# Kernel optimization log

Measured on AMD Instinct MI355X. Metric: run time of the kernel, lower is better.

## Reference

```python
import jax, jax.numpy as jnp
import numpy as np

N_USER = 100000
N_ITEM = 100000
N_EDGE = 1600000
IN_U = 128
IN_I = 128
OUT = 64
NEG_SLOPE = 0.01  # torch F.leaky_relu default


def setup_inputs() -> dict:
    key = jax.random.key(0)
    ks = jax.random.split(key, 12)
    return {
        'feat_user': jax.random.normal(ks[0], (N_USER, IN_U), jnp.float32),
        'feat_item': jax.random.normal(ks[1], (N_ITEM, IN_I), jnp.float32),
        'W_user': jax.random.normal(ks[2], (IN_U, OUT), jnp.float32) * 0.05,
        'b_user': jax.random.normal(ks[3], (OUT,), jnp.float32) * 0.05,
        'W_item': jax.random.normal(ks[4], (IN_I, OUT), jnp.float32) * 0.05,
        'b_item': jax.random.normal(ks[5], (OUT,), jnp.float32) * 0.05,
        'attn_w': jax.random.normal(ks[6], (2 * OUT, 1), jnp.float32) * 0.05,
        'src_u2i': jax.random.randint(ks[7], (N_EDGE,), 0, N_USER),
        'dst_u2i': jax.random.randint(ks[8], (N_EDGE,), 0, N_ITEM),
        'src_i2u': jax.random.randint(ks[9], (N_EDGE,), 0, N_ITEM),
        'dst_i2u': jax.random.randint(ks[10], (N_EDGE,), 0, N_USER),
    }


def _segment_softmax(e, seg, num_segments):
    # e: [E], seg: [E] destination ids -> softmax over edges sharing a dst
    m = jax.ops.segment_max(e, seg, num_segments=num_segments)
    ex = jnp.exp(e - m[seg])
    s = jax.ops.segment_sum(ex, seg, num_segments=num_segments)
    return ex / s[seg]


def _etype_aggregate(Wh_src, Wh_dst, attn_w, src, dst, n_dst):
    # gather per-edge src/dst projected features: [E, OUT]
    zs = Wh_src[src]
    zd = Wh_dst[dst]
    # attn([zs || zd]) == zs @ a_src + zd @ a_dst (split the 2*OUT weight)
    a_src, a_dst = attn_w[:OUT, 0], attn_w[OUT:, 0]
    e = zs @ a_src + zd @ a_dst  # [E]
    e = jnp.where(e > 0, e, NEG_SLOPE * e)  # leaky_relu
    alpha = _segment_softmax(e, dst, n_dst)  # [E]
    # weighted scatter-sum into destination nodes
    return jax.ops.segment_sum(alpha[:, None] * zs, dst, num_segments=n_dst)


def reference(feat_user, feat_item, W_user, b_user, W_item, b_item, attn_w,
              src_u2i, dst_u2i, src_i2u, dst_i2u):
    Wh_user = feat_user @ W_user + b_user  # fc['user'] (etype 'user': user->item)
    Wh_item = feat_item @ W_item + b_item  # fc['item'] (etype 'item': item->user)
    # etype 'user': user -> item; dst attention feature is Wh_item on item nodes
    h_item = _etype_aggregate(Wh_user, Wh_item, attn_w, src_u2i, dst_u2i, N_ITEM)
    # etype 'item': item -> user
    h_user = _etype_aggregate(Wh_item, Wh_user, attn_w, src_i2u, dst_i2u, N_USER)
    # update_nodes sums all 'self_*' per ntype; each ntype has exactly one here
    return jnp.concatenate([h_user, h_item], axis=0)  # [N_USER+N_ITEM, OUT]
```

## Files before the change

kernel.cpp:

```cpp
#include <hip/hip_runtime.h>
#include <hip/hip_bf16.h>

#define NU 100000
#define NI 100000
#define NE 1600000
#define KIN 128
#define KOUT 64

#define NCOPY 8
#define PBK 128
#define NP 782
#define CAP2 384
#define CHUNK 4096
#define SRTSZ (NCOPY * CAP2 + PBK * 7)
#define AGG_THREADS 512
#define NWAVE 8

#define LIN_ROWS 64
#define LIN_GRID 512
#define LIN_ITERS 1563

typedef short bf16x8 __attribute__((ext_vector_type(8)));
typedef float f32x4  __attribute__((ext_vector_type(4)));

__device__ __forceinline__ unsigned short f2bf(float f) {
    unsigned u = __float_as_uint(f);
    unsigned r = (u + 0x7fffu + ((u >> 16) & 1u)) >> 16;
    return (unsigned short)r;
}
__device__ __forceinline__ float bf2f(unsigned short h) {
    return __uint_as_float(((unsigned)h) << 16);
}
__device__ __forceinline__ void split_bf16(float f, unsigned short& h, unsigned short& l) {
    h = f2bf(f);
    float r = f - bf2f(h);
    l = f2bf(r);
}

__global__ __launch_bounds__(256) void linear_attn_kernel(
    const float* __restrict__ A0, const float* __restrict__ W0, const float* __restrict__ bv0,
    const float* __restrict__ A1, const float* __restrict__ W1, const float* __restrict__ bv1,
    const float* __restrict__ attn,
    unsigned short* __restrict__ Wh0, float* __restrict__ su0, float* __restrict__ sd0,
    unsigned short* __restrict__ Wh1, float* __restrict__ su1, float* __restrict__ sd1)
{
    __shared__ float Al[LIN_ROWS * 132];
    __shared__ __align__(16) unsigned short Wph[4 * 4 * 64 * 8];
    __shared__ __align__(16) unsigned short Wpl[4 * 4 * 64 * 8];

    int half = gridDim.x >> 1;
    bool second = blockIdx.x >= (unsigned)half;
    const float* A = second ? A1 : A0;
    const float* W = second ? W1 : W0;
    const float* bvec = second ? bv1 : bv0;
    unsigned short* Wh = second ? Wh1 : Wh0;
    float* s_src = second ? su1 : su0;
    float* s_dst = second ? sd1 : sd0;
    int blk = second ? (blockIdx.x - half) : blockIdx.x;

    int t = threadIdx.x;
    int l   = t & 63;
    int wv  = t >> 6;
    int ln  = l & 15;
    int grp = l >> 4;

    for (int i = 0; i < 4; i++) {
        int s = t + 256 * i;
        int sl = s & 63, nt = (s >> 6) & 3, ks = s >> 8;
        int kb = ks * 32 + (sl >> 4) * 8;
        int nn = nt * 16 + (sl & 15);
        int base = ((ks * 4 + nt) * 64 + sl) * 8;
        #pragma unroll
        for (int j = 0; j < 8; j++) {
            unsigned short h, lo2;
            split_bf16(W[(size_t)(kb + j) * KOUT + nn], h, lo2);
            Wph[base + j] = h; Wpl[base + j] = lo2;
        }
    }

    float asl[4], adl[4], bl4[4];
    #pragma unroll
    for (int nt = 0; nt < 4; nt++) {
        asl[nt] = attn[nt * 16 + ln];
        adl[nt] = attn[64 + nt * 16 + ln];
        bl4[nt] = bvec[nt * 16 + ln];
    }

    int arow = wv * 16 + ln;

    for (int c = blk; c < LIN_ITERS; c += half) {
        int rowbase = c * LIN_ROWS;
        __syncthreads();
        for (int g = t; g < LIN_ROWS * 32; g += 256) {
            int rr = g >> 5;
            int q  = g & 31;
            float4 v = {0.f, 0.f, 0.f, 0.f};
            int grow = rowbase + rr;
            if (grow < NU) v = ((const float4*)(A + (size_t)grow * 128))[q];
            *(float4*)&Al[rr * 132 + q * 4] = v;
        }
        __syncthreads();

        f32x4 acc0 = {bl4[0], bl4[0], bl4[0], bl4[0]};
        f32x4 acc1 = {bl4[1], bl4[1], bl4[1], bl4[1]};
        f32x4 acc2 = {bl4[2], bl4[2], bl4[2], bl4[2]};
        f32x4 acc3 = {bl4[3], bl4[3], bl4[3], bl4[3]};

        #pragma unroll
        for (int ks = 0; ks < 4; ks++) {
            int k0 = ks * 32 + grp * 8;
            const float* ap = &Al[arow * 132 + k0];
            float4 va = *(const float4*)ap;
            float4 vb = *(const float4*)(ap + 4);
            float av[8] = {va.x, va.y, va.z, va.w, vb.x, vb.y, vb.z, vb.w};
            bf16x8 ahi, alo;
            #pragma unroll
            for (int j = 0; j < 8; j++) {
                unsigned short h, lo2;
                split_bf16(av[j], h, lo2);
                ahi[j] = (short)h; alo[j] = (short)lo2;
            }
            #pragma unroll
            for (int nt = 0; nt < 4; nt++) {
                bf16x8 bhi8 = *(const bf16x8*)&Wph[((ks * 4 + nt) * 64 + l) * 8];
                bf16x8 blo8 = *(const bf16x8*)&Wpl[((ks * 4 + nt) * 64 + l) * 8];
                f32x4 a = (nt == 0) ? acc0 : (nt == 1) ? acc1 : (nt == 2) ? acc2 : acc3;
                a = __builtin_amdgcn_mfma_f32_16x16x32_bf16(ahi, bhi8, a, 0, 0, 0);
                a = __builtin_amdgcn_mfma_f32_16x16x32_bf16(ahi, blo8, a, 0, 0, 0);
                a = __builtin_amdgcn_mfma_f32_16x16x32_bf16(alo, bhi8, a, 0, 0, 0);
                if (nt == 0) acc0 = a; else if (nt == 1) acc1 = a; else if (nt == 2) acc2 = a; else acc3 = a;
            }
        }

        int growbase = rowbase + wv * 16;
        f32x4 accs[4] = {acc0, acc1, acc2, acc3};
        #pragma unroll
        for (int nt = 0; nt < 4; nt++) {
            #pragma unroll
            for (int r = 0; r < 4; r++) {
                int row = growbase + grp * 4 + r;
                if (row < NU) Wh[(size_t)row * KOUT + nt * 16 + ln] = f2bf(accs[nt][r]);
            }
        }
        #pragma unroll
        for (int r = 0; r < 4; r++) {
            float p1 = accs[0][r] * asl[0] + accs[1][r] * asl[1] + accs[2][r] * asl[2] + accs[3][r] * asl[3];
            float p2 = accs[0][r] * adl[0] + accs[1][r] * adl[1] + accs[2][r] * adl[2] + accs[3][r] * adl[3];
            #pragma unroll
            for (int off = 1; off < 16; off <<= 1) {
                p1 += __shfl_xor(p1, off);
                p2 += __shfl_xor(p2, off);
            }
            int row = growbase + grp * 4 + r;
            if (ln == 0 && row < NU) { s_src[row] = p1; s_dst[row] = p2; }
        }
    }
}

__global__ __launch_bounds__(256) void scatter_kernel(
    const int* __restrict__ src_u2i, const int* __restrict__ dst_u2i,
    const int* __restrict__ src_i2u, const int* __restrict__ dst_i2u,
    int* __restrict__ cur_item, int* __restrict__ cur_user,
    int* __restrict__ ebuf_item, int* __restrict__ ebuf_user,
    int nE, int nbs)
{
    __shared__ int raw[CHUNK];
    __shared__ unsigned short bkt[CHUNK];
    __shared__ int cnt[NP];
    __shared__ int gb[NP];
    __shared__ int lc[NP];

    bool u2i = blockIdx.x < (unsigned)nbs;
    int blk = u2i ? blockIdx.x : (blockIdx.x - nbs);
    int copy = blockIdx.x & (NCOPY - 1);
    const int* src = u2i ? src_u2i : src_i2u;
    const int* dst = u2i ? dst_u2i : dst_i2u;
    int* cur  = (u2i ? cur_item : cur_user) + copy * NP;
    int* ebuf = (u2i ? ebuf_item : ebuf_user) + (size_t)copy * NP * CAP2;

    int t = threadIdx.x;
    for (int i = t; i < NP; i += 256) { cnt[i] = 0; lc[i] = 0; }
    __syncthreads();

    int e0 = blk * CHUNK;
    int n = nE - e0; if (n > CHUNK) n = CHUNK;

    for (int j = t; j < n; j += 256) {
        int s = src[e0 + j], d = dst[e0 + j];
        int b = d >> 7;
        raw[j] = s | ((d & 127) << 17);
        bkt[j] = (unsigned short)b;
        atomicAdd(&cnt[b], 1);
    }
    __syncthreads();

    for (int b = t; b < NP; b += 256) {
        int c = cnt[b];
        gb[b] = c ? atomicAdd(&cur[b], c) : 0;
    }
    __syncthreads();

    for (int j = t; j < n; j += 256) {
        int b = bkt[j];
        int p = gb[b] + atomicAdd(&lc[b], 1);
        if (p < CAP2) ebuf[(size_t)b * CAP2 + p] = raw[j];
    }
}

__global__ __launch_bounds__(AGG_THREADS) void agg_kernel(
    const int* __restrict__ cur_item, const int* __restrict__ cur_user,
    const int* __restrict__ ebuf_item, const int* __restrict__ ebuf_user,
    const float* __restrict__ su_user, const float* __restrict__ sd_item,
    const float* __restrict__ su_item, const float* __restrict__ sd_user,
    const unsigned short* __restrict__ Wh_user, const unsigned short* __restrict__ Wh_item,
    float* __restrict__ h_item, float* __restrict__ h_user)
{
    __shared__ int   raw[SRTSZ];
    __shared__ int   srt[SRTSZ];
    __shared__ int   offs[NCOPY + 1];
    __shared__ int   cnt[PBK];
    __shared__ int   base[PBK + 1];
    __shared__ int   cursor[PBK];
    __shared__ float sdl[PBK];

    int bid = blockIdx.x;
    bool item_side = bid < NP;
    int b = item_side ? bid : bid - NP;
    const int*   cur  = item_side ? cur_item : cur_user;
    const int*   ebuf = item_side ? ebuf_item : ebuf_user;
    const float* ssrc = item_side ? su_user : su_item;
    const float* sdst = item_side ? sd_item : sd_user;
    const unsigned short* Whs = item_side ? Wh_user : Wh_item;
    float* h = item_side ? h_item : h_user;

    int t = threadIdx.x;
    if (t < PBK) {
        cnt[t] = 0;
        int node = b * PBK + t;
        sdl[t] = (node < NU) ? sdst[node] : 0.f;
    }
    if (t == 0) {
        int a = 0;
        #pragma unroll
        for (int c = 0; c < NCOPY; c++) {
            offs[c] = a;
            int cc = cur[c * NP + b];
            if (cc > CAP2) cc = CAP2;
            a += cc;
        }
        offs[NCOPY] = a;
    }
    for (int j = t; j < SRTSZ; j += AGG_THREADS) srt[j] = 0;
    __syncthreads();

    int total = offs[NCOPY];

    for (int j = t; j < total; j += AGG_THREADS) {
        int c = 0;
        while (j >= offs[c + 1]) c++;
        int e = ebuf[((size_t)c * NP + b) * CAP2 + (j - offs[c])];
        raw[j] = e;
        atomicAdd(&cnt[e >> 17], 1);
    }
    __syncthreads();

    if (t < 64) {
        int i0 = 2 * t, i1 = 2 * t + 1;
        int c0 = (cnt[i0] + 7) & ~7;
        int c1 = (cnt[i1] + 7) & ~7;
        int s = c0 + c1;
        int run = s;
        #pragma unroll
        for (int off = 1; off < 64; off <<= 1) {
            int v = __shfl_up(run, off);
            if (t >= off) run += v;
        }
        int excl = run - s;
        base[i0] = excl;      cursor[i0] = excl;
        base[i1] = excl + c0; cursor[i1] = excl + c0;
        if (t == 63) base[PBK] = run;
    }
    __syncthreads();

    for (int j = t; j < total; j += AGG_THREADS) {
        int e = raw[j];
        int p = atomicAdd(&cursor[e >> 17], 1);
        srt[p] = e;
    }
    __syncthreads();

    int lane = t & 63;
    int wv = t >> 6;

    float* wgt = (float*)raw;
    for (int dl = wv; dl < PBK; dl += NWAVE) {
        int jb = base[dl], cc = cnt[dl], pc = base[dl + 1] - jb;
        float sd = sdl[dl];
        for (int k = lane; k < pc; k += 64) {
            float w = 0.f;
            if (k < cc) {
                int s = srt[jb + k] & 0x1FFFF;
                float ev = ssrc[s] + sd;
                ev = ev > 0.f ? ev : 0.01f * ev;
                w = __expf(ev);
            }
            wgt[jb + k] = w;
        }
    }
    __syncthreads();

    int sub = lane >> 4;
    int ch4 = (lane & 15) << 2;
    const unsigned short* WhCh = Whs + ch4;
    for (int dl = wv; dl < PBK; dl += NWAVE) {
        int node = b * PBK + dl;
        if (node >= NU) break;
        int jb = base[dl];
        int pc = base[dl + 1] - jb;
        int cc = cnt[dl];
        float ax = 0.f, ay = 0.f, az = 0.f, aw = 0.f, ssum = 0.f;
        for (int q = 0; q < pc; q += 8) {
            int j0 = jb + q + sub;
            int j1 = j0 + 4;
            int e0 = srt[j0];
            int e1 = srt[j1];
            float w0 = wgt[j0];
            float w1 = wgt[j1];
            uint2 u0 = *(const uint2*)(WhCh + ((size_t)(e0 & 0x1FFFF) << 6));
            uint2 u1 = *(const uint2*)(WhCh + ((size_t)(e1 & 0x1FFFF) << 6));
            ax += w0 * __uint_as_float(u0.x << 16)         + w1 * __uint_as_float(u1.x << 16);
            ay += w0 * __uint_as_float(u0.x & 0xffff0000u) + w1 * __uint_as_float(u1.x & 0xffff0000u);
            az += w0 * __uint_as_float(u0.y << 16)         + w1 * __uint_as_float(u1.y << 16);
            aw += w0 * __uint_as_float(u0.y & 0xffff0000u) + w1 * __uint_as_float(u1.y & 0xffff0000u);
            ssum += w0 + w1;
        }
        #pragma unroll
        for (int off = 16; off <= 32; off <<= 1) {
            ax += __shfl_xor(ax, off);
            ay += __shfl_xor(ay, off);
            az += __shfl_xor(az, off);
            aw += __shfl_xor(aw, off);
            ssum += __shfl_xor(ssum, off);
        }
        if (sub == 0) {
            float inv = (cc > 0) ? 1.f / ssum : 0.f;
            float4 o = {ax * inv, ay * inv, az * inv, aw * inv};
            *(float4*)(h + (size_t)node * KOUT + ch4) = o;
        }
    }
}

extern "C" void kernel_launch(void* const* d_in, const int* in_sizes, int n_in,
                              void* d_out, int out_size, void* d_ws, size_t ws_size,
                              hipStream_t stream)
{
    const float* feat_user = (const float*)d_in[0];
    const float* feat_item = (const float*)d_in[1];
    const float* W_user    = (const float*)d_in[2];
    const float* b_user    = (const float*)d_in[3];
    const float* W_item    = (const float*)d_in[4];
    const float* b_item    = (const float*)d_in[5];
    const float* attn_w    = (const float*)d_in[6];
    const int*   src_u2i   = (const int*)d_in[7];
    const int*   dst_u2i   = (const int*)d_in[8];
    const int*   src_i2u   = (const int*)d_in[9];
    const int*   dst_i2u   = (const int*)d_in[10];

    float* out    = (float*)d_out;
    float* h_user = out;
    float* h_item = out + (size_t)NU * KOUT;

    char* p = (char*)d_ws;
    unsigned short* Wh_user = (unsigned short*)p; p += (size_t)NU * KOUT * 2;
    unsigned short* Wh_item = (unsigned short*)p; p += (size_t)NI * KOUT * 2;
    float* su_user = (float*)p; p += NU * 4;
    float* sd_user = (float*)p; p += NU * 4;
    float* su_item = (float*)p; p += NI * 4;
    float* sd_item = (float*)p; p += NI * 4;
    int* cur_item  = (int*)p; p += (size_t)NCOPY * NP * 4;
    int* cur_user  = (int*)p; p += (size_t)NCOPY * NP * 4;
    int* ebuf_item = (int*)p; p += (size_t)NCOPY * NP * CAP2 * 4;
    int* ebuf_user = (int*)p; p += (size_t)NCOPY * NP * CAP2 * 4;

    hipMemsetAsync(cur_item, 0, (size_t)2 * NCOPY * NP * 4, stream);

    int nbs = (NE + CHUNK - 1) / CHUNK;
    scatter_kernel<<<2 * nbs, 256, 0, stream>>>(src_u2i, dst_u2i, src_i2u, dst_i2u,
                                                cur_item, cur_user, ebuf_item, ebuf_user,
                                                NE, nbs);
    linear_attn_kernel<<<LIN_GRID, 256, 0, stream>>>(feat_user, W_user, b_user,
                                                     feat_item, W_item, b_item, attn_w,
                                                     Wh_user, su_user, sd_user,
                                                     Wh_item, su_item, sd_item);
    agg_kernel<<<2 * NP, AGG_THREADS, 0, stream>>>(cur_item, cur_user, ebuf_item, ebuf_user,
                                                   su_user, sd_item, su_item, sd_user,
                                                   Wh_user, Wh_item, h_item, h_user);
}
```

Before: 309.8 us.

## Keep W hi-part in registers, vectorize per-wave edge bucket loads, enlarge linear grid

The linear kernel now holds the bf16 high part of the weight tile in registers instead of LDS, which removes one LDS read per MFMA group and shrinks shared memory. The grid size goes from 512 to 768 blocks. In the aggregation kernel each wave loads its own copy bucket with int4 vector loads, replacing the per-element search over copy offsets. The trade-off is higher register pressure from 16 bf16x8 values per thread, and the vectorized path assumes 16-byte aligned bucket starts, which holds because CAP2 is a multiple of 4.

```diff
diff --git a/kernel.cpp b/kernel.cpp
--- a/kernel.cpp
+++ b/kernel.cpp
@@ -17,7 +17,7 @@
 #define NWAVE 8
 
 #define LIN_ROWS 64
-#define LIN_GRID 512
+#define LIN_GRID 768
 #define LIN_ITERS 1563
 
 typedef short bf16x8 __attribute__((ext_vector_type(8)));
@@ -45,7 +45,6 @@
     unsigned short* __restrict__ Wh1, float* __restrict__ su1, float* __restrict__ sd1)
 {
     __shared__ float Al[LIN_ROWS * 132];
-    __shared__ __align__(16) unsigned short Wph[4 * 4 * 64 * 8];
     __shared__ __align__(16) unsigned short Wpl[4 * 4 * 64 * 8];
 
     int half = gridDim.x >> 1;
@@ -64,17 +63,21 @@
     int ln  = l & 15;
     int grp = l >> 4;
 
-    for (int i = 0; i < 4; i++) {
-        int s = t + 256 * i;
-        int sl = s & 63, nt = (s >> 6) & 3, ks = s >> 8;
-        int kb = ks * 32 + (sl >> 4) * 8;
-        int nn = nt * 16 + (sl & 15);
-        int base = ((ks * 4 + nt) * 64 + sl) * 8;
-        #pragma unroll
-        for (int j = 0; j < 8; j++) {
-            unsigned short h, lo2;
-            split_bf16(W[(size_t)(kb + j) * KOUT + nn], h, lo2);
-            Wph[base + j] = h; Wpl[base + j] = lo2;
+    bf16x8 whi[4][4];
+    #pragma unroll
+    for (int ks = 0; ks < 4; ks++) {
+        #pragma unroll
+        for (int nt = 0; nt < 4; nt++) {
+            bf16x8 hi8, lo8;
+            #pragma unroll
+            for (int j = 0; j < 8; j++) {
+                float w = W[(size_t)(ks * 32 + grp * 8 + j) * KOUT + nt * 16 + ln];
+                unsigned short h, lo2;
+                split_bf16(w, h, lo2);
+                hi8[j] = (short)h; lo8[j] = (short)lo2;
+            }
+            whi[ks][nt] = hi8;
+            if (wv == 0) *(bf16x8*)&Wpl[((ks * 4 + nt) * 64 + l) * 8] = lo8;
         }
     }
 
@@ -122,12 +125,11 @@
             }
             #pragma unroll
             for (int nt = 0; nt < 4; nt++) {
-                bf16x8 bhi8 = *(const bf16x8*)&Wph[((ks * 4 + nt) * 64 + l) * 8];
                 bf16x8 blo8 = *(const bf16x8*)&Wpl[((ks * 4 + nt) * 64 + l) * 8];
                 f32x4 a = (nt == 0) ? acc0 : (nt == 1) ? acc1 : (nt == 2) ? acc2 : acc3;
-                a = __builtin_amdgcn_mfma_f32_16x16x32_bf16(ahi, bhi8, a, 0, 0, 0);
+                a = __builtin_amdgcn_mfma_f32_16x16x32_bf16(ahi, whi[ks][nt], a, 0, 0, 0);
                 a = __builtin_amdgcn_mfma_f32_16x16x32_bf16(ahi, blo8, a, 0, 0, 0);
-                a = __builtin_amdgcn_mfma_f32_16x16x32_bf16(alo, bhi8, a, 0, 0, 0);
+                a = __builtin_amdgcn_mfma_f32_16x16x32_bf16(alo, whi[ks][nt], a, 0, 0, 0);
                 if (nt == 0) acc0 = a; else if (nt == 1) acc1 = a; else if (nt == 2) acc2 = a; else acc3 = a;
             }
         }
@@ -234,6 +236,9 @@
     float* h = item_side ? h_item : h_user;
 
     int t = threadIdx.x;
+    int lane = t & 63;
+    int wv = t >> 6;
+
     if (t < PBK) {
         cnt[t] = 0;
         int node = b * PBK + t;
@@ -255,12 +260,26 @@
 
     int total = offs[NCOPY];
 
-    for (int j = t; j < total; j += AGG_THREADS) {
-        int c = 0;
-        while (j >= offs[c + 1]) c++;
-        int e = ebuf[((size_t)c * NP + b) * CAP2 + (j - offs[c])];
-        raw[j] = e;
-        atomicAdd(&cnt[e >> 17], 1);
+    {
+        int c = wv;
+        int jb = offs[c];
+        int cc = offs[c + 1] - jb;
+        const int* sp = ebuf + ((size_t)c * NP + b) * CAP2;
+        int nq = cc >> 2;
+        for (int k = lane; k < nq; k += 64) {
+            int4 v = *(const int4*)(sp + 4 * k);
+            int j = jb + 4 * k;
+            raw[j] = v.x; raw[j + 1] = v.y; raw[j + 2] = v.z; raw[j + 3] = v.w;
+            atomicAdd(&cnt[v.x >> 17], 1);
+            atomicAdd(&cnt[v.y >> 17], 1);
+            atomicAdd(&cnt[v.z >> 17], 1);
+            atomicAdd(&cnt[v.w >> 17], 1);
+        }
+        for (int k = (nq << 2) + lane; k < cc; k += 64) {
+            int e = sp[k];
+            raw[jb + k] = e;
+            atomicAdd(&cnt[e >> 17], 1);
+        }
     }
     __syncthreads();
 
@@ -288,9 +307,6 @@
         srt[p] = e;
     }
     __syncthreads();
-
-    int lane = t & 63;
-    int wv = t >> 6;
 
     float* wgt = (float*)raw;
     for (int dl = wv; dl < PBK; dl += NWAVE) {
```

Result: slower. 326.3 us (+5.4%).
